# Kernel tuning notes

Measured on AMD Instinct MI355X. Metric: run time of the kernel, lower is better.

The kernel has to match this reference:

```python
import jax, jax.numpy as jnp
import numpy as np

HID, HEADS, LAYERS = 64, 4, 2
D = HID // HEADS
NU, NE, NV = 30000, 60000, 1000
N_NODES = (NU, NE, NV)
OFFS = (0, NU, NU + NE, NU + NE + NV)
N_TOTAL = NU + NE + NV
# (src_type, dst_type, n_edges); node types: user=0, event=1, venue=2. Order matches module.edge_types.
EDGE_DEFS = (
    (0, 0, 150000),  # friend
    (0, 1, 120000), (0, 1, 60000), (0, 1, 40000), (0, 1, 30000), (0, 1, 50000),  # view/like/save/intent/attend
    (1, 0, 120000), (1, 0, 60000), (1, 0, 40000), (1, 0, 30000), (1, 0, 50000),  # rev_*
    (1, 2, 60000),  # hosted_at
    (2, 1, 60000),  # hosts
)
EDGE_NAMES = ('ei_friend', 'ei_view', 'ei_like', 'ei_save', 'ei_intent', 'ei_attend',
              'ei_rev_view', 'ei_rev_like', 'ei_rev_save', 'ei_rev_intent', 'ei_rev_attend',
              'ei_hosted_at', 'ei_hosts')


def _l2norm(x):
    return x / jnp.maximum(jnp.linalg.norm(x, axis=-1, keepdims=True), 1e-12)


def _hgt_layer(h, edges, Wkqv, bkqv, Wk, Wv, p_rel, Wout, bout, skip):
    # h: list of per-node-type features [N_t, HID]. Fused K/Q/V projection per node type.
    kqv = [h[t] @ Wkqv[t] + bkqv[t] for t in range(3)]  # [N_t, 3*HID]
    k = [a[:, :HID].reshape(-1, HEADS, D) for a in kqv]
    q = [a[:, HID:2 * HID].reshape(-1, HEADS, D) for a in kqv]
    v = [a[:, 2 * HID:].reshape(-1, HEADS, D) for a in kqv]
    scale = 1.0 / np.sqrt(D).astype(np.float32)
    scores, msgs, dsts = [], [], []
    for e, (s, d, _) in enumerate(EDGE_DEFS):
        src_idx, dst_idx = edges[e][0], edges[e][1]
        # per-(edge_type, head) DxD relation transforms (PyG k_rel / v_rel)
        ke = jnp.einsum('nhd,hde->nhe', k[s], Wk[e])[src_idx]  # [E,H,D]
        ve = jnp.einsum('nhd,hde->nhe', v[s], Wv[e])[src_idx]  # [E,H,D]
        qi = q[d][dst_idx]                                      # [E,H,D]
        scores.append((qi * ke).sum(-1) * p_rel[e] * scale)     # [E,H]
        msgs.append(ve)
        dsts.append(dst_idx + OFFS[d])
    sc = jnp.concatenate(scores)   # [E_tot, H]
    ms = jnp.concatenate(msgs)     # [E_tot, H, D]
    dst = jnp.concatenate(dsts)    # [E_tot] global destination ids
    # destination-grouped softmax across all edge types jointly
    smax = jax.lax.stop_gradient(jax.ops.segment_max(sc, dst, num_segments=N_TOTAL))
    ex = jnp.exp(sc - smax[dst])
    den = jax.ops.segment_sum(ex, dst, num_segments=N_TOTAL)
    alpha = ex / den[dst]
    agg = jax.ops.segment_sum(alpha[:, :, None] * ms, dst, num_segments=N_TOTAL).reshape(N_TOTAL, HID)
    out = []
    for t in range(3):
        o = agg[OFFS[t]:OFFS[t + 1]]
        a = jax.nn.gelu(o, approximate=False) @ Wout[t] + bout[t]
        g = jax.nn.sigmoid(skip[t])  # learnable skip gate
        out.append(g * a + (1.0 - g) * h[t])
    return out


def _forward(x_user, x_event, x_venue, W_user, b_user, W_event, b_event, W_venue, b_venue,
             emb_user, emb_event, emb_venue, Wkqv, bkqv, Wk, Wv, p_rel, Wout, bout, skip,
             ids_user, ids_event, ids_venue, edges):
    h = [x_user @ W_user + b_user + emb_user[ids_user],
         x_event @ W_event + b_event + emb_event[ids_event],
         x_venue @ W_venue + b_venue + emb_venue[ids_venue]]
    for l in range(LAYERS):
        h = _hgt_layer(h, edges, Wkqv[l], bkqv[l], Wk[l], Wv[l], p_rel[l], Wout[l], bout[l], skip[l])
        h = [jax.nn.relu(x) for x in h]  # dropout is identity in eval mode
    return tuple(_l2norm(x) for x in h)


def setup_inputs() -> dict:
    key = jax.random.key(0)
    ks = iter(jax.random.split(key, 64))
    s = 0.05
    inp = {
        'x_user': jax.random.normal(next(ks), (NU, 32), jnp.float32),
        'x_event': jax.random.normal(next(ks), (NE, 32), jnp.float32),
        'x_venue': jax.random.normal(next(ks), (NV, 16), jnp.float32),
        'W_user': jax.random.normal(next(ks), (32, HID), jnp.float32) * s,
        'b_user': jnp.zeros((HID,), jnp.float32),
        'W_event': jax.random.normal(next(ks), (32, HID), jnp.float32) * s,
        'b_event': jnp.zeros((HID,), jnp.float32),
        'W_venue': jax.random.normal(next(ks), (16, HID), jnp.float32) * s,
        'b_venue': jnp.zeros((HID,), jnp.float32),
        'emb_user': jax.random.normal(next(ks), (NU, HID), jnp.float32) * s,
        'emb_event': jax.random.normal(next(ks), (NE, HID), jnp.float32) * s,
        'emb_venue': jax.random.normal(next(ks), (NV, HID), jnp.float32) * s,
        'Wkqv': jax.random.normal(next(ks), (LAYERS, 3, HID, 3 * HID), jnp.float32) * s,
        'bkqv': jnp.zeros((LAYERS, 3, 3 * HID), jnp.float32),
        'Wk': jax.random.normal(next(ks), (LAYERS, 13, HEADS, D, D), jnp.float32) * 0.2,
        'Wv': jax.random.normal(next(ks), (LAYERS, 13, HEADS, D, D), jnp.float32) * 0.2,
        'p_rel': jnp.ones((LAYERS, 13, HEADS), jnp.float32),
        'Wout': jax.random.normal(next(ks), (LAYERS, 3, HID, HID), jnp.float32) * s,
        'bout': jnp.zeros((LAYERS, 3, HID), jnp.float32),
        'skip': jnp.ones((LAYERS, 3), jnp.float32),
        'ids_user': jnp.arange(NU, dtype=jnp.int32),
        'ids_event': jnp.arange(NE, dtype=jnp.int32),
        'ids_venue': jnp.arange(NV, dtype=jnp.int32),
    }
    for name, (st, dt, n) in zip(EDGE_NAMES, EDGE_DEFS):
        src = jax.random.randint(next(ks), (n,), 0, N_NODES[st], dtype=jnp.int32)
        dst = jax.random.randint(next(ks), (n,), 0, N_NODES[dt], dtype=jnp.int32)
        inp[name] = jnp.stack([src, dst])
    return inp


def reference(x_user, x_event, x_venue, W_user, b_user, W_event, b_event, W_venue, b_venue,
              emb_user, emb_event, emb_venue, Wkqv, bkqv, Wk, Wv, p_rel, Wout, bout, skip,
              ids_user, ids_event, ids_venue,
              ei_friend, ei_view, ei_like, ei_save, ei_intent, ei_attend,
              ei_rev_view, ei_rev_like, ei_rev_save, ei_rev_intent, ei_rev_attend,
              ei_hosted_at, ei_hosts):
    edges = (ei_friend, ei_view, ei_like, ei_save, ei_intent, ei_attend,
             ei_rev_view, ei_rev_like, ei_rev_save, ei_rev_intent, ei_rev_attend,
             ei_hosted_at, ei_hosts)
    return _forward(x_user, x_event, x_venue, W_user, b_user, W_event, b_event, W_venue, b_venue,
                    emb_user, emb_event, emb_venue, Wkqv, bkqv, Wk, Wv, p_rel, Wout, bout, skip,
                    ids_user, ids_event, ids_venue, edges)
```

## Files before the change

### kernel.cpp

```cpp
#include <hip/hip_runtime.h>
#include <hip/hip_fp16.h>
#include <math.h>

#define HID   64
#define HEADS 4
#define DH    16
#define NU    30000
#define NE_   60000
#define NV    1000
#define NTOT  91000
#define ETOT  870000
#define NSLOT 541000
#define LAYERS 2

__device__ const int d_EOFF[14] = {0,150000,270000,330000,370000,400000,450000,
                                   570000,630000,670000,700000,750000,810000,870000};
__device__ const int d_ECNT[13] = {150000,120000,60000,40000,30000,50000,
                                   120000,60000,40000,30000,50000,60000,60000};
__device__ const int d_EST[13]  = {0,0,0,0,0,0,1,1,1,1,1,1,2};
__device__ const int d_EDT[13]  = {0,1,1,1,1,1,0,0,0,0,0,2,1};
__device__ const int d_NOFF[3]  = {0, NU, NU + NE_};
__device__ const int d_EBASE[13] = {0,30000,60000,90000,120000,150000,
                                    180000,240000,300000,360000,420000,480000,540000};

struct EdgePtrs { const int* p[13]; };

typedef float f32x2 __attribute__((ext_vector_type(2)));

__device__ __forceinline__ void pk_fma(f32x2& acc, f32x2 a, f32x2 b) {
    asm("v_pk_fma_f32 %0, %1, %2, %0" : "+v"(acc) : "v"(a), "v"(b));
}
__device__ __forceinline__ void pk_fma_sv(f32x2& acc, f32x2 a_sgpr, f32x2 b) {
    asm("v_pk_fma_f32 %0, %1, %2, %0" : "+v"(acc) : "s"(a_sgpr), "v"(b));
}

__device__ __forceinline__ int node_type(int n) {
    return (n >= NU) + (n >= NU + NE_);
}

__global__ __launch_bounds__(64)
void k_init(const float* __restrict__ xu, const float* __restrict__ xe,
            const float* __restrict__ xv,
            const float* __restrict__ Wu, const float* __restrict__ bu,
            const float* __restrict__ We, const float* __restrict__ be,
            const float* __restrict__ Wv_, const float* __restrict__ bv,
            const float* __restrict__ embu, const float* __restrict__ embe,
            const float* __restrict__ embv,
            const int* __restrict__ idu, const int* __restrict__ ide,
            const int* __restrict__ idv,
            float* __restrict__ h) {
    int n0 = blockIdx.x * 16;
    int t = node_type(n0);
    int j = threadIdx.x;
    const float *x, *W, *bb, *emb; const int* ids; int in_dim;
    if (t == 0)      { x = xu; W = Wu;  bb = bu; emb = embu; ids = idu; in_dim = 32; }
    else if (t == 1) { x = xe; W = We;  bb = be; emb = embe; ids = ide; in_dim = 32; }
    else             { x = xv; W = Wv_; bb = bv; emb = embv; ids = idv; in_dim = 16; }
    int nl = n0 - d_NOFF[t];
    int nn = min(16, NTOT - n0);
    __shared__ float xT[32][20];
    int ncs = (in_dim == 32) ? 3 : 2;
    int nch = 1 << ncs;
    for (int idx = j; idx < (nch << 4); idx += 64) {
        int n = idx >> ncs, c = idx & (nch - 1);
        float4 v = make_float4(0.f, 0.f, 0.f, 0.f);
        if (n < nn) v = *(const float4*)(x + (size_t)(nl + n) * in_dim + c * 4);
        xT[c * 4 + 0][n] = v.x;
        xT[c * 4 + 1][n] = v.y;
        xT[c * 4 + 2][n] = v.z;
        xT[c * 4 + 3][n] = v.w;
    }
    __syncthreads();
    float bj = bb[j];
    f32x2 acc2[8];
    #pragma unroll
    for (int p = 0; p < 8; p++) {
        float ex = (2 * p     < nn) ? emb[(size_t)ids[nl + 2 * p    ] * 64 + j] : 0.f;
        float ey = (2 * p + 1 < nn) ? emb[(size_t)ids[nl + 2 * p + 1] * 64 + j] : 0.f;
        acc2[p].x = bj + ex; acc2[p].y = bj + ey;
    }
    if (in_dim == 32) {
        #pragma unroll
        for (int i = 0; i < 32; i++) {
            float w = W[i * 64 + j];
            f32x2 w2; w2.x = w; w2.y = w;
            #pragma unroll
            for (int qd = 0; qd < 4; qd++) {
                float4 hv = *(const float4*)(&xT[i][qd * 4]);
                f32x2 p0; p0.x = hv.x; p0.y = hv.y; pk_fma(acc2[2 * qd],     p0, w2);
                f32x2 p1; p1.x = hv.z; p1.y = hv.w; pk_fma(acc2[2 * qd + 1], p1, w2);
            }
        }
    } else {
        #pragma unroll
        for (int i = 0; i < 16; i++) {
            float w = W[i * 64 + j];
            f32x2 w2; w2.x = w; w2.y = w;
            #pragma unroll
            for (int qd = 0; qd < 4; qd++) {
                float4 hv = *(const float4*)(&xT[i][qd * 4]);
                f32x2 p0; p0.x = hv.x; p0.y = hv.y; pk_fma(acc2[2 * qd],     p0, w2);
                f32x2 p1; p1.x = hv.z; p1.y = hv.w; pk_fma(acc2[2 * qd + 1], p1, w2);
            }
        }
    }
    #pragma unroll
    for (int p = 0; p < 8; p++) {
        if (2 * p     < nn) h[(size_t)(n0 + 2 * p)     * 64 + j] = acc2[p].x;
        if (2 * p + 1 < nn) h[(size_t)(n0 + 2 * p + 1) * 64 + j] = acc2[p].y;
    }
}

__global__ void k_cnt(EdgePtrs ep, int* __restrict__ cnt, int* __restrict__ pos) {
    int eidx = blockIdx.x * blockDim.x + threadIdx.x;
    if (eidx >= ETOT) return;
    int e = 0;
    #pragma unroll
    for (int i = 1; i < 13; i++) e += (eidx >= d_EOFF[i]);
    int li = eidx - d_EOFF[e];
    int dst = ep.p[e][d_ECNT[e] + li];
    pos[eidx] = atomicAdd(&cnt[d_NOFF[d_EDT[e]] + dst], 1);
}

__global__ void k_scan_a(const int* __restrict__ cnt, int* __restrict__ partial) {
    __shared__ int s[256];
    int i = blockIdx.x * 256 + threadIdx.x;
    s[threadIdx.x] = (i < NTOT) ? cnt[i] : 0;
    __syncthreads();
    for (int off = 128; off > 0; off >>= 1) {
        if (threadIdx.x < off) s[threadIdx.x] += s[threadIdx.x + off];
        __syncthreads();
    }
    if (threadIdx.x == 0) partial[blockIdx.x] = s[0];
}

__global__ void k_scan_b(int* __restrict__ partial, int nblk) {
    __shared__ int s[512];
    int t = threadIdx.x;
    s[t] = (t < nblk) ? partial[t] : 0;
    __syncthreads();
    for (int off = 1; off < 512; off <<= 1) {
        int v = (t >= off) ? s[t - off] : 0;
        __syncthreads();
        s[t] += v;
        __syncthreads();
    }
    if (t < nblk) partial[t] = t ? s[t - 1] : 0;
}

__global__ void k_scan_c(const int* __restrict__ cnt, const int* __restrict__ partial,
                         int* __restrict__ row_ptr) {
    __shared__ int s[256];
    int i = blockIdx.x * 256 + threadIdx.x, t = threadIdx.x;
    int v = (i < NTOT) ? cnt[i] : 0;
    s[t] = v;
    __syncthreads();
    for (int off = 1; off < 256; off <<= 1) {
        int u = (t >= off) ? s[t - off] : 0;
        __syncthreads();
        s[t] += u;
        __syncthreads();
    }
    if (i < NTOT) row_ptr[i] = s[t] - v + partial[blockIdx.x];
    if (i == NTOT - 1) row_ptr[NTOT] = s[t] + partial[blockIdx.x];
}

__global__ void k_fill(EdgePtrs ep, const int* __restrict__ row_ptr,
                       const int* __restrict__ pos, int* __restrict__ csr) {
    int eidx = blockIdx.x * blockDim.x + threadIdx.x;
    if (eidx >= ETOT) return;
    int e = 0;
    #pragma unroll
    for (int i = 1; i < 13; i++) e += (eidx >= d_EOFF[i]);
    int li = eidx - d_EOFF[e];
    const int* base = ep.p[e];
    int src = base[li], dst = base[d_ECNT[e] + li];
    int dg = d_NOFF[d_EDT[e]] + dst;
    csr[row_ptr[dg] + pos[eidx]] = d_EBASE[e] + src;
}

__global__ __launch_bounds__(192, 3)
void k_kqvt(const float* __restrict__ h, const float* __restrict__ Wkqv,
            const float* __restrict__ bkqv, const float* __restrict__ Wk,
            const float* __restrict__ Wv, const float* __restrict__ prel,
            float* __restrict__ qagg, __half2* __restrict__ kvt, int layer) {
    int n0 = blockIdx.x * 16;
    int t = node_type(n0);
    __shared__ float kq[16][192];
    int j = threadIdx.x;

    const float* hb = h + (size_t)n0 * 64;
    const float* Wc = Wkqv + (size_t)(layer * 3 + t) * HID * 192 + j;
    float b = bkqv[(layer * 3 + t) * 192 + j];
    f32x2 acc2[16];
    #pragma unroll
    for (int n = 0; n < 16; n++) { acc2[n].x = 0.f; acc2[n].y = 0.f; }
    #pragma unroll
    for (int ic = 0; ic < 16; ic++) {
        float w0 = Wc[(size_t)(4 * ic + 0) * 192];
        float w1 = Wc[(size_t)(4 * ic + 1) * 192];
        float w2 = Wc[(size_t)(4 * ic + 2) * 192];
        float w3 = Wc[(size_t)(4 * ic + 3) * 192];
        f32x2 wA; wA.x = w0; wA.y = w1;
        f32x2 wB; wB.x = w2; wB.y = w3;
        #pragma unroll
        for (int n = 0; n < 16; n++) {
            float4 hv = *(const float4*)(hb + n * 64 + ic * 4);
            f32x2 p0; p0.x = hv.x; p0.y = hv.y;
            pk_fma_sv(acc2[n], p0, wA);
            f32x2 p1; p1.x = hv.z; p1.y = hv.w;
            pk_fma_sv(acc2[n], p1, wB);
        }
    }
    float accf[16];
    #pragma unroll
    for (int n = 0; n < 16; n++) accf[n] = b + acc2[n].x + acc2[n].y;
    #pragma unroll
    for (int n = 0; n < 16; n++) kq[n][j] = accf[n];
    if (j >= 64 && j < 128) {
        #pragma unroll
        for (int n = 0; n < 16; n++)
            if (n0 + n < NTOT) qagg[(size_t)(n0 + n) * 64 + (j - 64)] = accf[n];
    }
    __syncthreads();

    int wave = j >> 6, lane = j & 63;
    int hh = lane >> 4, xo = lane & 15;
    int ne = (t == 2) ? 1 : 6;
    int e0 = (t == 0) ? 0 : (t == 1) ? 6 : 12;
    int eA = e0 + wave, eB = e0 + wave + 3;
    bool vA = wave < ne, vB = wave + 3 < ne;
    int nt = n0 - d_NOFF[t];
    f32x2 wkA[8], wvA[8], wkB[8], wvB[8];
    int sbA = 0, sbB = 0;
    if (vA) {
        const float* Wkp = Wk + (((size_t)layer * 13 + eA) * 4 + hh) * 256 + xo;
        const float* Wvp = Wv + (((size_t)layer * 13 + eA) * 4 + hh) * 256 + xo;
        float pr = prel[(layer * 13 + eA) * 4 + hh] * 0.25f;
        #pragma unroll
        for (int p = 0; p < 8; p++) {
            wkA[p].x = Wkp[(2 * p)     * 16] * pr;
            wkA[p].y = Wkp[(2 * p + 1) * 16] * pr;
            wvA[p].x = Wvp[(2 * p)     * 16];
            wvA[p].y = Wvp[(2 * p + 1) * 16];
        }
        sbA = d_EBASE[eA] + nt;
    }
    if (vB) {
        const float* Wkp = Wk + (((size_t)layer * 13 + eB) * 4 + hh) * 256 + xo;
        const float* Wvp = Wv + (((size_t)layer * 13 + eB) * 4 + hh) * 256 + xo;
        float pr = prel[(layer * 13 + eB) * 4 + hh] * 0.25f;
        #pragma unroll
        for (int p = 0; p < 8; p++) {
            wkB[p].x = Wkp[(2 * p)     * 16] * pr;
            wkB[p].y = Wkp[(2 * p + 1) * 16] * pr;
            wvB[p].x = Wvp[(2 * p)     * 16];
            wvB[p].y = Wvp[(2 * p + 1) * 16];
        }
        sbB = d_EBASE[eB] + nt;
    }
    #pragma unroll
    for (int n = 0; n < 16; n++) {
        bool ok = (n0 + n) < NTOT;
        const float* kr = &kq[n][hh * 16];
        const float* vr = &kq[n][128 + hh * 16];
        float4 k0 = ((const float4*)kr)[0];
        float4 k1 = ((const float4*)kr)[1];
        float4 k2 = ((const float4*)kr)[2];
        float4 k3 = ((const float4*)kr)[3];
        float4 v0 = ((const float4*)vr)[0];
        float4 v1 = ((const float4*)vr)[1];
        float4 v2 = ((const float4*)vr)[2];
        float4 v3 = ((const float4*)vr)[3];
        if (vA & ok) {
            f32x2 ak; ak.x = 0.f; ak.y = 0.f;
            f32x2 av; av.x = 0.f; av.y = 0.f;
            f32x2 p0;
            p0.x = k0.x; p0.y = k0.y; pk_fma(ak, p0, wkA[0]);
            p0.x = k0.z; p0.y = k0.w; pk_fma(ak, p0, wkA[1]);
            p0.x = k1.x; p0.y = k1.y; pk_fma(ak, p0, wkA[2]);
            p0.x = k1.z; p0.y = k1.w; pk_fma(ak, p0, wkA[3]);
            p0.x = k2.x; p0.y = k2.y; pk_fma(ak, p0, wkA[4]);
            p0.x = k2.z; p0.y = k2.w; pk_fma(ak, p0, wkA[5]);
            p0.x = k3.x; p0.y = k3.y; pk_fma(ak, p0, wkA[6]);
            p0.x = k3.z; p0.y = k3.w; pk_fma(ak, p0, wkA[7]);
            p0.x = v0.x; p0.y = v0.y; pk_fma(av, p0, wvA[0]);
            p0.x = v0.z; p0.y = v0.w; pk_fma(av, p0, wvA[1]);
            p0.x = v1.x; p0.y = v1.y; pk_fma(av, p0, wvA[2]);
            p0.x = v1.z; p0.y = v1.w; pk_fma(av, p0, wvA[3]);
            p0.x = v2.x; p0.y = v2.y; pk_fma(av, p0, wvA[4]);
            p0.x = v2.z; p0.y = v2.w; pk_fma(av, p0, wvA[5]);
            p0.x = v3.x; p0.y = v3.y; pk_fma(av, p0, wvA[6]);
            p0.x = v3.z; p0.y = v3.w; pk_fma(av, p0, wvA[7]);
            float kt = ak.x + ak.y;
            float vt = av.x + av.y;
            kvt[(size_t)(sbA + n) * 64 + lane] = __float22half2_rn(make_float2(kt, vt));
        }
        if (vB & ok) {
            f32x2 ak; ak.x = 0.f; ak.y = 0.f;
            f32x2 av; av.x = 0.f; av.y = 0.f;
            f32x2 p0;
            p0.x = k0.x; p0.y = k0.y; pk_fma(ak, p0, wkB[0]);
            p0.x = k0.z; p0.y = k0.w; pk_fma(ak, p0, wkB[1]);
            p0.x = k1.x; p0.y = k1.y; pk_fma(ak, p0, wkB[2]);
            p0.x = k1.z; p0.y = k1.w; pk_fma(ak, p0, wkB[3]);
            p0.x = k2.x; p0.y = k2.y; pk_fma(ak, p0, wkB[4]);
            p0.x = k2.z; p0.y = k2.w; pk_fma(ak, p0, wkB[5]);
            p0.x = k3.x; p0.y = k3.y; pk_fma(ak, p0, wkB[6]);
            p0.x = k3.z; p0.y = k3.w; pk_fma(ak, p0, wkB[7]);
            p0.x = v0.x; p0.y = v0.y; pk_fma(av, p0, wvB[0]);
            p0.x = v0.z; p0.y = v0.w; pk_fma(av, p0, wvB[1]);
            p0.x = v1.x; p0.y = v1.y; pk_fma(av, p0, wvB[2]);
            p0.x = v1.z; p0.y = v1.w; pk_fma(av, p0, wvB[3]);
            p0.x = v2.x; p0.y = v2.y; pk_fma(av, p0, wvB[4]);
            p0.x = v2.z; p0.y = v2.w; pk_fma(av, p0, wvB[5]);
            p0.x = v3.x; p0.y = v3.y; pk_fma(av, p0, wvB[6]);
            p0.x = v3.z; p0.y = v3.w; pk_fma(av, p0, wvB[7]);
            float kt = ak.x + ak.y;
            float vt = av.x + av.y;
            kvt[(size_t)(sbB + n) * 64 + lane] = __float22half2_rn(make_float2(kt, vt));
        }
    }
}

__device__ __forceinline__ float row_sum16(float x) {
    int v;
    v = __builtin_amdgcn_update_dpp(0, __float_as_int(x), 0xB1, 0xF, 0xF, true);
    x += __int_as_float(v);
    v = __builtin_amdgcn_update_dpp(0, __float_as_int(x), 0x4E, 0xF, 0xF, true);
    x += __int_as_float(v);
    v = __builtin_amdgcn_update_dpp(0, __float_as_int(x), 0x141, 0xF, 0xF, true);
    x += __int_as_float(v);
    v = __builtin_amdgcn_update_dpp(0, __float_as_int(x), 0x140, 0xF, 0xF, true);
    x += __int_as_float(v);
    return x;
}

__device__ __forceinline__ void osm_step(float s, float vv,
                                         float& m, float& l, float& acc) {
    float d = s - m;
    float t = __expf(-fabsf(d));
    bool pos = d > 0.f;
    m = fmaxf(m, s);
    float sc = pos ? t : 1.f;
    float es = pos ? 1.f : t;
    l   = l * sc + es;
    acc = acc * sc + es * vv;
}

__global__ __launch_bounds__(512, 4)
void k_gather(const float* __restrict__ qagg, const __half2* __restrict__ kvt,
              const int* __restrict__ row_ptr, const int* __restrict__ csr,
              const float* __restrict__ Wout, const float* __restrict__ bout,
              const float* __restrict__ skip,
              float* __restrict__ h, float* __restrict__ out,
              int layer, int last) {
    int wave = threadIdx.x >> 6, lane = threadIdx.x & 63;
    int node = blockIdx.x * 8 + wave;
    int t = node_type(node);
    float hprev = h[(size_t)node * 64 + lane];
    float bb = bout[(layer * 3 + t) * 64 + lane];
    float gk = 1.f / (1.f + __expf(-skip[layer * 3 + t]));
    float q = qagg[(size_t)node * 64 + lane];
    int beg = row_ptr[node], end = row_ptr[node + 1];
    float m0 = -1e30f, l0 = 0.f, a0 = 0.f;
    float m1 = -1e30f, l1 = 0.f, a1 = 0.f;
    float m2 = -1e30f, l2 = 0.f, a2 = 0.f;
    float m3 = -1e30f, l3 = 0.f, a3 = 0.f;
    for (int base = beg; base < end; base += 64) {
        int n = end - base; if (n > 64) n = 64;
        int ent = csr[base + ((lane < n) ? lane : 0)];
        for (int c = 0; c < n; c += 8) {
            int cn = n - c; if (cn > 8) cn = 8;
            __half2 f[8];
            #pragma unroll
            for (int k = 0; k < 8; k++) {
                int idx = c + ((k < cn) ? k : 0);
                int sl = __shfl(ent, idx, 64);
                f[k] = kvt[(size_t)sl * 64 + lane];
            }
            float s8[8];
            #pragma unroll
            for (int k = 0; k < 8; k++) {
                if (k >= cn) break;
                s8[k] = row_sum16(q * __low2float(f[k]));
            }
            if (0 < cn) osm_step(s8[0], __high2float(f[0]), m0, l0, a0);
            if (1 < cn) osm_step(s8[1], __high2float(f[1]), m1, l1, a1);
            if (2 < cn) osm_step(s8[2], __high2float(f[2]), m2, l2, a2);
            if (3 < cn) osm_step(s8[3], __high2float(f[3]), m3, l3, a3);
            if (4 < cn) osm_step(s8[4], __high2float(f[4]), m0, l0, a0);
            if (5 < cn) osm_step(s8[5], __high2float(f[5]), m1, l1, a1);
            if (6 < cn) osm_step(s8[6], __high2float(f[6]), m2, l2, a2);
            if (7 < cn) osm_step(s8[7], __high2float(f[7]), m3, l3, a3);
        }
    }
    float M   = fmaxf(fmaxf(m0, m1), fmaxf(m2, m3));
    float e0  = __expf(m0 - M), e1 = __expf(m1 - M);
    float e2  = __expf(m2 - M), e3 = __expf(m3 - M);
    float l   = l0 * e0 + l1 * e1 + l2 * e2 + l3 * e3;
    float acc = a0 * e0 + a1 * e1 + a2 * e2 + a3 * e3;
    float og  = (l > 0.f) ? acc / l : 0.f;

    float gl = 0.5f * og * (1.f + erff(og * 0.70710678118654752f));
    __shared__ float gs[8][64];
    gs[wave][lane] = gl;
    const float* W = Wout + (size_t)(layer * 3 + t) * 4096 + lane;
    const float* gsp = &gs[wave][0];
    f32x2 a2v; a2v.x = bb; a2v.y = 0.f;
    #pragma unroll
    for (int i4 = 0; i4 < 16; i4++) {
        float4 g4 = *(const float4*)(gsp + i4 * 4);
        float w0 = W[(size_t)(i4 * 4 + 0) * 64];
        float w1 = W[(size_t)(i4 * 4 + 1) * 64];
        float w2 = W[(size_t)(i4 * 4 + 2) * 64];
        float w3 = W[(size_t)(i4 * 4 + 3) * 64];
        f32x2 p0; p0.x = g4.x; p0.y = g4.y;
        f32x2 q0; q0.x = w0;  q0.y = w1;
        pk_fma(a2v, p0, q0);
        f32x2 p1; p1.x = g4.z; p1.y = g4.w;
        f32x2 q1; q1.x = w2;  q1.y = w3;
        pk_fma(a2v, p1, q1);
    }
    float r = gk * (a2v.x + a2v.y) + (1.f - gk) * hprev;
    r = fmaxf(r, 0.f);
    if (!last) {
        h[(size_t)node * 64 + lane] = r;
    } else {
        float ss = r * r;
        ss += __shfl_xor(ss, 1, 64);  ss += __shfl_xor(ss, 2, 64);
        ss += __shfl_xor(ss, 4, 64);  ss += __shfl_xor(ss, 8, 64);
        ss += __shfl_xor(ss, 16, 64); ss += __shfl_xor(ss, 32, 64);
        float nrm = fmaxf(sqrtf(ss), 1e-12f);
        out[(size_t)node * 64 + lane] = r / nrm;
    }
}

extern "C" void kernel_launch(void* const* d_in, const int* in_sizes, int n_in,
                              void* d_out, int out_size, void* d_ws, size_t ws_size,
                              hipStream_t stream) {
    const float* xu   = (const float*)d_in[0];
    const float* xe   = (const float*)d_in[1];
    const float* xv   = (const float*)d_in[2];
    const float* Wu   = (const float*)d_in[3];
    const float* bu   = (const float*)d_in[4];
    const float* We   = (const float*)d_in[5];
    const float* be   = (const float*)d_in[6];
    const float* Wv_  = (const float*)d_in[7];
    const float* bv   = (const float*)d_in[8];
    const float* embu = (const float*)d_in[9];
    const float* embe = (const float*)d_in[10];
    const float* embv = (const float*)d_in[11];
    const float* Wkqv = (const float*)d_in[12];
    const float* bkqv = (const float*)d_in[13];
    const float* Wk   = (const float*)d_in[14];
    const float* Wv   = (const float*)d_in[15];
    const float* prel = (const float*)d_in[16];
    const float* Wout = (const float*)d_in[17];
    const float* bout = (const float*)d_in[18];
    const float* skip = (const float*)d_in[19];
    const int*   idu  = (const int*)d_in[20];
    const int*   ide  = (const int*)d_in[21];
    const int*   idv  = (const int*)d_in[22];
    EdgePtrs ep;
    for (int e = 0; e < 13; e++) ep.p[e] = (const int*)d_in[23 + e];

    float* ws  = (float*)d_ws;
    float* h      = ws;
    float* qagg   = h    + (size_t)NTOT * HID;
    __half2* kvt  = (__half2*)(qagg + (size_t)NTOT * HID);
    int* cnt     = (int*)(kvt + (size_t)NSLOT * HID);
    int* row_ptr = cnt + NTOT;
    int* partial = row_ptr + NTOT + 1;
    int* csr     = partial + 512;
    int* pos     = csr + ETOT;

    k_init<<<(NTOT + 15) / 16, 64, 0, stream>>>(
        xu, xe, xv, Wu, bu, We, be, Wv_, bv, embu, embe, embv, idu, ide, idv, h);

    hipMemsetAsync(cnt, 0, (size_t)NTOT * 4, stream);
    int nblk = (NTOT + 255) / 256;
    k_cnt<<<(ETOT + 255) / 256, 256, 0, stream>>>(ep, cnt, pos);
    k_scan_a<<<nblk, 256, 0, stream>>>(cnt, partial);
    k_scan_b<<<1, 512, 0, stream>>>(partial, nblk);
    k_scan_c<<<nblk, 256, 0, stream>>>(cnt, partial, row_ptr);
    k_fill<<<(ETOT + 255) / 256, 256, 0, stream>>>(ep, row_ptr, pos, csr);

    for (int l = 0; l < LAYERS; l++) {
        k_kqvt<<<(NTOT + 15) / 16, 192, 0, stream>>>(h, Wkqv, bkqv, Wk, Wv, prel,
                                                     qagg, kvt, l);
        k_gather<<<NTOT / 8, 512, 0, stream>>>(qagg, kvt, row_ptr, csr,
                                               Wout, bout, skip, h,
                                               (float*)d_out, l, l == LAYERS - 1);
    }
}
```

Before: 628.2 us.

## Split output projection across waves with shared-memory partial sums

Before, each wave did the full 64x64 output matvec for its own node and read all 64 weight rows per lane. Now the 8 waves in a block share their GELU activations through transposed shared memory. Each wave applies 8 weight rows to all 8 nodes, and the partial sums are reduced through a second shared buffer. This cuts per-wave weight loads eightfold. The cost is two block barriers and extra LDS traffic, and the code assumes every wave in a block reaches the barriers and uses the same node type's weights.

```diff
diff --git a/kernel.cpp b/kernel.cpp
--- a/kernel.cpp
+++ b/kernel.cpp
@@ -403,26 +403,37 @@
     float og  = (l > 0.f) ? acc / l : 0.f;
 
     float gl = 0.5f * og * (1.f + erff(og * 0.70710678118654752f));
-    __shared__ float gs[8][64];
-    gs[wave][lane] = gl;
-    const float* W = Wout + (size_t)(layer * 3 + t) * 4096 + lane;
-    const float* gsp = &gs[wave][0];
-    f32x2 a2v; a2v.x = bb; a2v.y = 0.f;
-    #pragma unroll
-    for (int i4 = 0; i4 < 16; i4++) {
-        float4 g4 = *(const float4*)(gsp + i4 * 4);
-        float w0 = W[(size_t)(i4 * 4 + 0) * 64];
-        float w1 = W[(size_t)(i4 * 4 + 1) * 64];
-        float w2 = W[(size_t)(i4 * 4 + 2) * 64];
-        float w3 = W[(size_t)(i4 * 4 + 3) * 64];
-        f32x2 p0; p0.x = g4.x; p0.y = g4.y;
-        f32x2 q0; q0.x = w0;  q0.y = w1;
-        pk_fma(a2v, p0, q0);
-        f32x2 p1; p1.x = g4.z; p1.y = g4.w;
-        f32x2 q1; q1.x = w2;  q1.y = w3;
-        pk_fma(a2v, p1, q1);
-    }
-    float r = gk * (a2v.x + a2v.y) + (1.f - gk) * hprev;
+    __shared__ float gsT[64][12];
+    __shared__ float part[8][8][64];
+    gsT[lane][wave] = gl;
+    __syncthreads();
+    const float* Wb = Wout + (size_t)(layer * 3 + t) * 4096 + lane;
+    f32x2 acc2[4];
+    #pragma unroll
+    for (int p = 0; p < 4; p++) { acc2[p].x = 0.f; acc2[p].y = 0.f; }
+    #pragma unroll
+    for (int ii = 0; ii < 8; ii++) {
+        int i = wave * 8 + ii;
+        float w = Wb[(size_t)i * 64];
+        f32x2 w2; w2.x = w; w2.y = w;
+        const float* gr = &gsT[i][0];
+        float4 ga = *(const float4*)(gr);
+        float4 gb = *(const float4*)(gr + 4);
+        f32x2 p0; p0.x = ga.x; p0.y = ga.y; pk_fma(acc2[0], p0, w2);
+        f32x2 p1; p1.x = ga.z; p1.y = ga.w; pk_fma(acc2[1], p1, w2);
+        f32x2 p2; p2.x = gb.x; p2.y = gb.y; pk_fma(acc2[2], p2, w2);
+        f32x2 p3; p3.x = gb.z; p3.y = gb.w; pk_fma(acc2[3], p3, w2);
+    }
+    #pragma unroll
+    for (int p = 0; p < 4; p++) {
+        part[wave][2 * p][lane]     = acc2[p].x;
+        part[wave][2 * p + 1][lane] = acc2[p].y;
+    }
+    __syncthreads();
+    float s = bb;
+    #pragma unroll
+    for (int gg = 0; gg < 8; gg++) s += part[gg][wave][lane];
+    float r = gk * s + (1.f - gk) * hprev;
     r = fmaxf(r, 0.f);
     if (!last) {
         h[(size_t)node * 64 + lane] = r;
```

Result: faster. 582.9 us (median of 2 runs) (-7.2%).
